# Kernel tuning notes

Hardware: AMD Instinct MI355X
Metric: run time of the kernel (lower is better)

Reference implementation:

```python
import jax, jax.numpy as jnp
import numpy as np

N_NODES = 100000
N_EDGES = 1600000
HID = 256
HEADS = 4
HEAD_DIM = HID // HEADS
EPS = 1e-5


def _layernorm(x, g, b):
    mu = jnp.mean(x, axis=-1, keepdims=True)
    var = jnp.mean(jnp.square(x - mu), axis=-1, keepdims=True)
    return (x - mu) * jax.lax.rsqrt(var + EPS) * g + b


def setup_inputs() -> dict:
    key = jax.random.key(0)
    ks = jax.random.split(key, 16)
    s = 0.05  # small init, mimics xavier gain=0.1
    inp = {
        'h': jax.random.normal(ks[0], (N_NODES, HID), jnp.float32),
        'src': jax.random.randint(ks[1], (N_EDGES,), 0, N_NODES, jnp.int32),
        'dst': jax.random.randint(ks[2], (N_EDGES,), 0, N_NODES, jnp.int32),
        'Wq': jax.random.normal(ks[3], (HID, HID), jnp.float32) * s,
        'bq': jnp.zeros((HID,), jnp.float32),
        'Wk': jax.random.normal(ks[4], (HID, HID), jnp.float32) * s,
        'bk': jnp.zeros((HID,), jnp.float32),
        'Wv': jax.random.normal(ks[5], (HID, HID), jnp.float32) * s,
        'bv': jnp.zeros((HID,), jnp.float32),
        'Wo': jax.random.normal(ks[6], (HID, HID), jnp.float32) * s,
        'bo': jnp.zeros((HID,), jnp.float32),
        'W1': jax.random.normal(ks[7], (HID, 2 * HID), jnp.float32) * s,
        'b1': jnp.zeros((2 * HID,), jnp.float32),
        'W2': jax.random.normal(ks[8], (2 * HID, HID), jnp.float32) * s,
        'b2': jnp.zeros((HID,), jnp.float32),
        'g1': jnp.ones((HID,), jnp.float32),
        'be1': jnp.zeros((HID,), jnp.float32),
        'g2': jnp.ones((HID,), jnp.float32),
        'be2': jnp.zeros((HID,), jnp.float32),
    }
    return inp


def reference(h, src, dst, Wq, bq, Wk, bk, Wv, bv, Wo, bo, W1, b1, W2, b2, g1, be1, g2, be2):
    N = h.shape[0]
    scale = HEAD_DIM ** -0.5
    h_norm = _layernorm(h, g1, be1)
    Q = (h_norm @ Wq + bq).reshape(N, HEADS, HEAD_DIM)
    K = (h_norm @ Wk + bk).reshape(N, HEADS, HEAD_DIM)
    V = (h_norm @ Wv + bv).reshape(N, HEADS, HEAD_DIM)

    # per-edge attention logits: q from dst, k from src  -> [E, heads]
    logits = jnp.einsum('ehd,ehd->eh', Q[dst], K[src]) * scale

    # edge softmax grouped by destination node (dgl.ops.edge_softmax)
    seg_max = jax.ops.segment_max(logits, dst, num_segments=N)  # [N, heads]
    e = jnp.exp(logits - seg_max[dst])
    seg_sum = jax.ops.segment_sum(e, dst, num_segments=N)
    w = e / seg_sum[dst]  # [E, heads]

    # message = V[src] * attn ; aggregate by sum over incoming edges
    msg = V[src] * w[:, :, None]  # [E, heads, head_dim]
    h_new = jax.ops.segment_sum(msg, dst, num_segments=N).reshape(N, HID)

    h_attn = h_new @ Wo + bo
    h = h + h_attn  # dropout is identity in eval
    h2 = _layernorm(h, g2, be2)
    ffn = jax.nn.relu(h2 @ W1 + b1) @ W2 + b2
    return h + ffn
```

## Files before the change

### kernel.cpp

```cpp
#include <hip/hip_runtime.h>
#include <hip/hip_bf16.h>

#define NN 100000
#define NE 1600000

typedef __attribute__((ext_vector_type(8))) short bf16x8;
typedef __attribute__((ext_vector_type(4))) float f32x4;
typedef __attribute__((ext_vector_type(2))) float f32x2;
typedef __attribute__((ext_vector_type(2))) unsigned int u32x2;
typedef __attribute__((ext_vector_type(4))) unsigned int u32x4;

__device__ __forceinline__ float bf2f(unsigned short u) {
    union { unsigned int i; float f; } c; c.i = ((unsigned int)u) << 16; return c.f;
}
__device__ __forceinline__ unsigned short f2bf(float f) {
    union { float f; unsigned int i; } c; c.f = f;
    unsigned int lsb = (c.i >> 16) & 1u;
    c.i += 0x7FFFu + lsb;
    return (unsigned short)(c.i >> 16);
}
__device__ __forceinline__ unsigned char f2fp8(float v) {
    return (unsigned char)(__builtin_amdgcn_cvt_pk_fp8_f32(v, v, 0, false) & 0xff);
}
__device__ __forceinline__ void gload_lds16(const void* g, void* l) {
    __builtin_amdgcn_global_load_lds(
        (const __attribute__((address_space(1))) void*)g,
        (__attribute__((address_space(3))) void*)l, 16, 0, 0);
}

__global__ __launch_bounds__(256) void ln_k(
    const float* __restrict__ x, const float* __restrict__ g,
    const float* __restrict__ b, unsigned short* __restrict__ y, int nrows)
{
    int w = threadIdx.x >> 6, lane = threadIdx.x & 63;
    int row = blockIdx.x * 4 + w;
    if (row >= nrows) return;
    const float4 xv = *(const float4*)(x + (size_t)row * 256 + lane * 4);
    float s  = xv.x + xv.y + xv.z + xv.w;
    float sq = xv.x*xv.x + xv.y*xv.y + xv.z*xv.z + xv.w*xv.w;
    #pragma unroll
    for (int m = 1; m < 64; m <<= 1) {
        s  += __shfl_xor(s,  m);
        sq += __shfl_xor(sq, m);
    }
    float mu  = s * (1.0f / 256.0f);
    float var = sq * (1.0f / 256.0f) - mu * mu;
    float r = rsqrtf(var + 1e-5f);
    float4 gv = *(const float4*)(g + lane * 4);
    float4 bv = *(const float4*)(b + lane * 4);
    ushort4 o;
    o.x = f2bf((xv.x - mu) * r * gv.x + bv.x);
    o.y = f2bf((xv.y - mu) * r * gv.y + bv.y);
    o.z = f2bf((xv.z - mu) * r * gv.z + bv.z);
    o.w = f2bf((xv.w - mu) * r * gv.w + bv.w);
    *(ushort4*)(y + (size_t)row * 256 + lane * 4) = o;
}

__global__ __launch_bounds__(256) void wconv_k(
    const float* __restrict__ W, unsigned short* __restrict__ Wt, int K, int N)
{
    __shared__ unsigned short tl[32][33];
    int bk = blockIdx.x * 32, bn = blockIdx.y * 32;
    int lx = threadIdx.x & 31, ly = threadIdx.x >> 5;
    #pragma unroll
    for (int r = 0; r < 32; r += 8)
        tl[ly + r][lx] = f2bf(W[(size_t)(bk + ly + r) * N + bn + lx]);
    __syncthreads();
    #pragma unroll
    for (int r = 0; r < 32; r += 8)
        Wt[(size_t)(bn + ly + r) * K + bk + lx] = tl[lx][ly + r];
}

__global__ void bcat_k(const float* __restrict__ a, const float* __restrict__ b,
                       const float* __restrict__ c, float* __restrict__ o)
{
    int t = threadIdx.x;
    o[t] = a[t]; o[256 + t] = b[t]; o[512 + t] = c[t];
}

template<int OMODE, bool RELU, bool RES>
__global__ __launch_bounds__(512) void mgemm_k(
    const unsigned short* __restrict__ A, const unsigned short* __restrict__ Wt,
    const float* __restrict__ bias, void* __restrict__ outv, void* __restrict__ out2,
    const float* __restrict__ res, int M, int N, int K)
{
    __shared__ __align__(16) char lds[49152];
    const int t = threadIdx.x;
    const int lane = t & 63;
    const int wid = t >> 6;
    const int wm = wid >> 2, wn = wid & 3;
    const int bm = blockIdx.y * 128, bn = blockIdx.x * 256;

    f32x4 acc[4][4] = {};

    const int ra_s = t >> 2;
    const int sa_s = (t & 3) ^ (ra_s & 3);
    const size_t arow = (size_t)min(bm + ra_s, M - 1) * K + sa_s * 8;
    const int rb0 = t >> 2;
    const int sb0 = (t & 3) ^ (rb0 & 3);
    const int rb1 = (512 + t) >> 2;
    const int sb1 = (t & 3) ^ (rb1 & 3);
    const size_t brow0 = (size_t)(bn + rb0) * K + sb0 * 8;
    const size_t brow1 = (size_t)(bn + rb1) * K + sb1 * 8;

    const int fr = lane & 15, fs = lane >> 4;
    const int rslot = fs ^ (fr & 3);

    const int KS = K >> 5;
    int cur = 0;
    {
        unsigned short* Ab = (unsigned short*)(lds);
        unsigned short* Bb = (unsigned short*)(lds + 16384);
        gload_lds16(A + arow, Ab + t * 8);
        gload_lds16(Wt + brow0, Bb + t * 8);
        gload_lds16(Wt + brow1, Bb + (512 + t) * 8);
    }
    for (int ks = 0; ks < KS; ++ks) {
        __syncthreads();
        if (ks + 1 < KS) {
            int k1 = (ks + 1) << 5;
            unsigned short* Ab = (unsigned short*)(lds + (cur ^ 1) * 8192);
            unsigned short* Bb = (unsigned short*)(lds + 16384 + (cur ^ 1) * 16384);
            gload_lds16(A + arow + k1, Ab + t * 8);
            gload_lds16(Wt + brow0 + k1, Bb + t * 8);
            gload_lds16(Wt + brow1 + k1, Bb + (512 + t) * 8);
        }
        const unsigned short* As = (const unsigned short*)(lds + cur * 8192);
        const unsigned short* Bs = (const unsigned short*)(lds + 16384 + cur * 16384);
        bf16x8 af[4], bf[4];
        #pragma unroll
        for (int fm = 0; fm < 4; ++fm)
            af[fm] = *(const bf16x8*)&As[(wm * 64 + fm * 16 + fr) * 32 + rslot * 8];
        #pragma unroll
        for (int fn = 0; fn < 4; ++fn)
            bf[fn] = *(const bf16x8*)&Bs[(wn * 64 + fn * 16 + fr) * 32 + rslot * 8];
        #pragma unroll
        for (int fm = 0; fm < 4; ++fm)
            #pragma unroll
            for (int fn = 0; fn < 4; ++fn)
                acc[fm][fn] = __builtin_amdgcn_mfma_f32_16x16x32_bf16(
                    af[fm], bf[fn], acc[fm][fn], 0, 0, 0);
        cur ^= 1;
    }
    __syncthreads();

    float* wl = (float*)(lds + wid * 4352);
    const int rr = lane >> 2;
    const int c4 = (lane & 3) * 16;
    const int qg = lane >> 4;
    #pragma unroll
    for (int fm = 0; fm < 4; ++fm) {
        #pragma unroll
        for (int fn = 0; fn < 4; ++fn)
            #pragma unroll
            for (int i = 0; i < 4; ++i)
                wl[(qg * 4 + i) * 68 + fn * 16 + fr] = acc[fm][fn][i];
        f32x4 v0 = *(const f32x4*)&wl[rr * 68 + c4 + 0];
        f32x4 v1 = *(const f32x4*)&wl[rr * 68 + c4 + 4];
        f32x4 v2 = *(const f32x4*)&wl[rr * 68 + c4 + 8];
        f32x4 v3 = *(const f32x4*)&wl[rr * 68 + c4 + 12];
        const int rowg = bm + wm * 64 + fm * 16 + rr;
        const int colg = bn + wn * 64 + c4;
        if (rowg < M) {
            f32x4 b0 = *(const f32x4*)&bias[colg + 0];
            f32x4 b1 = *(const f32x4*)&bias[colg + 4];
            f32x4 b2 = *(const f32x4*)&bias[colg + 8];
            f32x4 b3 = *(const f32x4*)&bias[colg + 12];
            v0 += b0; v1 += b1; v2 += b2; v3 += b3;
            if (RES) {
                const float* rp = res + (size_t)rowg * N + colg;
                v0 += *(const f32x4*)(rp + 0);
                v1 += *(const f32x4*)(rp + 4);
                v2 += *(const f32x4*)(rp + 8);
                v3 += *(const f32x4*)(rp + 12);
            }
            if (RELU) {
                #pragma unroll
                for (int j = 0; j < 4; ++j) {
                    v0[j] = fmaxf(v0[j], 0.f); v1[j] = fmaxf(v1[j], 0.f);
                    v2[j] = fmaxf(v2[j], 0.f); v3[j] = fmaxf(v3[j], 0.f);
                }
            }
            if (OMODE == 0) {
                float* op = (float*)outv + (size_t)rowg * N + colg;
                *(f32x4*)(op + 0) = v0; *(f32x4*)(op + 4) = v1;
                *(f32x4*)(op + 8) = v2; *(f32x4*)(op + 12) = v3;
            } else if (OMODE == 1) {
                unsigned short* op = (unsigned short*)outv + (size_t)rowg * N + colg;
                u32x4 pa, pb;
                pa.x = f2bf(v0[0]) | ((unsigned int)f2bf(v0[1]) << 16);
                pa.y = f2bf(v0[2]) | ((unsigned int)f2bf(v0[3]) << 16);
                pa.z = f2bf(v1[0]) | ((unsigned int)f2bf(v1[1]) << 16);
                pa.w = f2bf(v1[2]) | ((unsigned int)f2bf(v1[3]) << 16);
                pb.x = f2bf(v2[0]) | ((unsigned int)f2bf(v2[1]) << 16);
                pb.y = f2bf(v2[2]) | ((unsigned int)f2bf(v2[3]) << 16);
                pb.z = f2bf(v3[0]) | ((unsigned int)f2bf(v3[1]) << 16);
                pb.w = f2bf(v3[2]) | ((unsigned int)f2bf(v3[3]) << 16);
                *(u32x4*)(op + 0) = pa;
                *(u32x4*)(op + 8) = pb;
            } else {
                if (colg < 256) {
                    unsigned short* op = (unsigned short*)outv + (size_t)rowg * 256 + colg;
                    u32x4 pa, pb;
                    pa.x = f2bf(v0[0]) | ((unsigned int)f2bf(v0[1]) << 16);
                    pa.y = f2bf(v0[2]) | ((unsigned int)f2bf(v0[3]) << 16);
                    pa.z = f2bf(v1[0]) | ((unsigned int)f2bf(v1[1]) << 16);
                    pa.w = f2bf(v1[2]) | ((unsigned int)f2bf(v1[3]) << 16);
                    pb.x = f2bf(v2[0]) | ((unsigned int)f2bf(v2[1]) << 16);
                    pb.y = f2bf(v2[2]) | ((unsigned int)f2bf(v2[3]) << 16);
                    pb.z = f2bf(v3[0]) | ((unsigned int)f2bf(v3[1]) << 16);
                    pb.w = f2bf(v3[2]) | ((unsigned int)f2bf(v3[3]) << 16);
                    *(u32x4*)(op + 0) = pa;
                    *(u32x4*)(op + 8) = pb;
                } else {
                    u32x4 p8;
                    unsigned int w0, w1, w2, w3;
                    w0 = __builtin_amdgcn_cvt_pk_fp8_f32(v0[0], v0[1], 0, false);
                    w0 = __builtin_amdgcn_cvt_pk_fp8_f32(v0[2], v0[3], w0, true);
                    w1 = __builtin_amdgcn_cvt_pk_fp8_f32(v1[0], v1[1], 0, false);
                    w1 = __builtin_amdgcn_cvt_pk_fp8_f32(v1[2], v1[3], w1, true);
                    w2 = __builtin_amdgcn_cvt_pk_fp8_f32(v2[0], v2[1], 0, false);
                    w2 = __builtin_amdgcn_cvt_pk_fp8_f32(v2[2], v2[3], w2, true);
                    w3 = __builtin_amdgcn_cvt_pk_fp8_f32(v3[0], v3[1], 0, false);
                    w3 = __builtin_amdgcn_cvt_pk_fp8_f32(v3[2], v3[3], w3, true);
                    p8.x = w0; p8.y = w1; p8.z = w2; p8.w = w3;
                    *(u32x4*)((unsigned char*)out2 + (size_t)rowg * 512 + (colg - 256)) = p8;
                }
            }
        }
    }
}

__global__ void degcnt_k(const int* __restrict__ dst, int* __restrict__ deg, int E)
{
    int e = blockIdx.x * blockDim.x + threadIdx.x;
    if (e < E) atomicAdd(deg + dst[e], 1);
}

__global__ __launch_bounds__(1024) void scan_k(int* __restrict__ a, int n)
{
    __shared__ int wsum[16];
    __shared__ int carry;
    __shared__ int tot;
    int t = threadIdx.x, lane = t & 63, w = t >> 6;
    if (t == 0) carry = 0;
    __syncthreads();
    for (int base = 0; base < n; base += 1024) {
        int i = base + t;
        int v = (i < n) ? a[i] : 0;
        int s = v;
        #pragma unroll
        for (int d2 = 1; d2 < 64; d2 <<= 1) {
            int u = __shfl_up(s, d2);
            if (lane >= d2) s += u;
        }
        if (lane == 63) wsum[w] = s;
        __syncthreads();
        if (t == 0) {
            int run = 0;
            #pragma unroll
            for (int j = 0; j < 16; ++j) { int x = wsum[j]; wsum[j] = run; run += x; }
            tot = run;
        }
        __syncthreads();
        int excl = carry + wsum[w] + (s - v);
        if (i < n) a[i] = excl;
        __syncthreads();
        if (t == 0) carry += tot;
        __syncthreads();
    }
    if (threadIdx.x == 0) a[n] = carry;
}

__global__ void scatter_k(
    const int* __restrict__ dst, const int* __restrict__ srcarr,
    const int* __restrict__ off, int* __restrict__ cursor,
    int* __restrict__ csr, int E)
{
    int e = blockIdx.x * blockDim.x + threadIdx.x;
    if (e >= E) return;
    int d = dst[e];
    int pos = off[d] + atomicAdd(cursor + d, 1);
    csr[pos] = srcarr[e];
}

__global__ __launch_bounds__(256) void attn_k(
    const int* __restrict__ csr, const int* __restrict__ off,
    const unsigned short* __restrict__ Q, const unsigned char* __restrict__ KV8,
    unsigned short* __restrict__ hnew)
{
    int w = threadIdx.x >> 6, lane = threadIdx.x & 63;
    int n = blockIdx.x * 4 + w;
    if (n >= NN) return;
    int e0 = off[n], e1 = off[n + 1];

    u32x2 qr = __builtin_nontemporal_load((const u32x2*)(Q + (size_t)n * 256 + lane * 4));
    const float q0 = bf2f((unsigned short)(qr.x & 0xffff)) * 0.125f;
    const float q1 = bf2f((unsigned short)(qr.x >> 16))    * 0.125f;
    const float q2 = bf2f((unsigned short)(qr.y & 0xffff)) * 0.125f;
    const float q3 = bf2f((unsigned short)(qr.y >> 16))    * 0.125f;

    float s = 0.f;
    float a0 = 0.f, a1 = 0.f, a2 = 0.f, a3 = 0.f;

    int i = e0;
    for (; i + 7 < e1; i += 8) {
        int ns[8];
        #pragma unroll
        for (int j = 0; j < 8; ++j) ns[j] = csr[i + j];
        unsigned int kd[8], vd[8];
        #pragma unroll
        for (int j = 0; j < 8; ++j) {
            const unsigned char* r = KV8 + (size_t)ns[j] * 512 + lane * 4;
            kd[j] = *(const unsigned int*)r;
            vd[j] = *(const unsigned int*)(r + 256);
        }
        float l[8];
        #pragma unroll
        for (int j = 0; j < 8; ++j) {
            f32x2 ka = __builtin_amdgcn_cvt_pk_f32_fp8(kd[j], false);
            f32x2 kb = __builtin_amdgcn_cvt_pk_f32_fp8(kd[j], true);
            l[j] = q0 * ka.x + q1 * ka.y + q2 * kb.x + q3 * kb.y;
        }
        #pragma unroll
        for (int m2 = 1; m2 < 16; m2 <<= 1) {
            #pragma unroll
            for (int j = 0; j < 8; ++j) l[j] += __shfl_xor(l[j], m2);
        }
        #pragma unroll
        for (int j = 0; j < 8; ++j) {
            float p = __expf(l[j]);
            f32x2 va = __builtin_amdgcn_cvt_pk_f32_fp8(vd[j], false);
            f32x2 vb = __builtin_amdgcn_cvt_pk_f32_fp8(vd[j], true);
            s  += p;
            a0 += p * va.x; a1 += p * va.y;
            a2 += p * vb.x; a3 += p * vb.y;
        }
    }
    for (; i + 3 < e1; i += 4) {
        int ns[4];
        #pragma unroll
        for (int j = 0; j < 4; ++j) ns[j] = csr[i + j];
        unsigned int kd[4], vd[4];
        #pragma unroll
        for (int j = 0; j < 4; ++j) {
            const unsigned char* r = KV8 + (size_t)ns[j] * 512 + lane * 4;
            kd[j] = *(const unsigned int*)r;
            vd[j] = *(const unsigned int*)(r + 256);
        }
        float l[4];
        #pragma unroll
        for (int j = 0; j < 4; ++j) {
            f32x2 ka = __builtin_amdgcn_cvt_pk_f32_fp8(kd[j], false);
            f32x2 kb = __builtin_amdgcn_cvt_pk_f32_fp8(kd[j], true);
            l[j] = q0 * ka.x + q1 * ka.y + q2 * kb.x + q3 * kb.y;
        }
        #pragma unroll
        for (int m2 = 1; m2 < 16; m2 <<= 1) {
            #pragma unroll
            for (int j = 0; j < 4; ++j) l[j] += __shfl_xor(l[j], m2);
        }
        #pragma unroll
        for (int j = 0; j < 4; ++j) {
            float p = __expf(l[j]);
            f32x2 va = __builtin_amdgcn_cvt_pk_f32_fp8(vd[j], false);
            f32x2 vb = __builtin_amdgcn_cvt_pk_f32_fp8(vd[j], true);
            s  += p;
            a0 += p * va.x; a1 += p * va.y;
            a2 += p * vb.x; a3 += p * vb.y;
        }
    }
    for (; i < e1; ++i) {
        int n0 = csr[i];
        const unsigned char* r = KV8 + (size_t)n0 * 512 + lane * 4;
        unsigned int kd = *(const unsigned int*)r;
        unsigned int vd = *(const unsigned int*)(r + 256);
        f32x2 ka = __builtin_amdgcn_cvt_pk_f32_fp8(kd, false);
        f32x2 kb = __builtin_amdgcn_cvt_pk_f32_fp8(kd, true);
        float l0 = q0 * ka.x + q1 * ka.y + q2 * kb.x + q3 * kb.y;
        #pragma unroll
        for (int m2 = 1; m2 < 16; m2 <<= 1) l0 += __shfl_xor(l0, m2);
        float p = __expf(l0);
        f32x2 va = __builtin_amdgcn_cvt_pk_f32_fp8(vd, false);
        f32x2 vb = __builtin_amdgcn_cvt_pk_f32_fp8(vd, true);
        s  += p;
        a0 += p * va.x; a1 += p * va.y;
        a2 += p * vb.x; a3 += p * vb.y;
    }
    float inv = (e1 > e0) ? 1.0f / s : 0.f;
    u32x2 ov;
    ov.x = ((unsigned int)f2bf(a1 * inv) << 16) | f2bf(a0 * inv);
    ov.y = ((unsigned int)f2bf(a3 * inv) << 16) | f2bf(a2 * inv);
    __builtin_nontemporal_store(ov, (u32x2*)(hnew + (size_t)n * 256 + lane * 4));
}

extern "C" void kernel_launch(void* const* d_in, const int* in_sizes, int n_in,
                              void* d_out, int out_size, void* d_ws, size_t ws_size,
                              hipStream_t stream)
{
    if (n_in < 19) return;
    const float* h   = (const float*)d_in[0];
    const int*   src = (const int*)d_in[1];
    const int*   dst = (const int*)d_in[2];
    const float* Wq  = (const float*)d_in[3];
    const float* bq  = (const float*)d_in[4];
    const float* Wk  = (const float*)d_in[5];
    const float* bk  = (const float*)d_in[6];
    const float* Wv  = (const float*)d_in[7];
    const float* bv  = (const float*)d_in[8];
    const float* Wo  = (const float*)d_in[9];
    const float* bo  = (const float*)d_in[10];
    const float* W1  = (const float*)d_in[11];
    const float* b1  = (const float*)d_in[12];
    const float* W2  = (const float*)d_in[13];
    const float* b2  = (const float*)d_in[14];
    const float* g1  = (const float*)d_in[15];
    const float* be1 = (const float*)d_in[16];
    const float* g2  = (const float*)d_in[17];
    const float* be2 = (const float*)d_in[18];
    float* out = (float*)d_out;

    char* w = (char*)d_ws;
    unsigned short* hnormb = (unsigned short*)(w + 0);
    unsigned short* Qb     = (unsigned short*)(w + 51200000);
    unsigned char*  KV8    = (unsigned char*)(w + 102400000);
    int*            degoff = (int*)(w + 153600000);
    int*            cursor = (int*)(w + 154000384);
    int*            csr    = (int*)(w + 154400768);
    unsigned short* Wqkvt  = (unsigned short*)(w + 160800768);
    unsigned short* Wot    = (unsigned short*)(w + 161193984);
    unsigned short* W1t    = (unsigned short*)(w + 161325056);
    unsigned short* W2t    = (unsigned short*)(w + 161587200);
    float*          bqkv   = (float*)(w + 161849344);
    unsigned short* hnewb  = hnormb;
    unsigned short* h2nb   = hnormb;
    unsigned short* ffnmid = (unsigned short*)(w + 51200000);

    hipMemsetAsync(degoff, 0, 400384, stream);
    hipMemsetAsync(cursor, 0, 400384, stream);

    const int M = NN;
    dim3 blk(256);
    dim3 blk512(512);

    wconv_k<<<dim3(8, 8),  blk, 0, stream>>>(Wq, Wqkvt,             256, 256);
    wconv_k<<<dim3(8, 8),  blk, 0, stream>>>(Wk, Wqkvt + 256 * 256, 256, 256);
    wconv_k<<<dim3(8, 8),  blk, 0, stream>>>(Wv, Wqkvt + 512 * 256, 256, 256);
    wconv_k<<<dim3(8, 8),  blk, 0, stream>>>(Wo, Wot, 256, 256);
    wconv_k<<<dim3(8, 16), blk, 0, stream>>>(W1, W1t, 256, 512);
    wconv_k<<<dim3(16, 8), blk, 0, stream>>>(W2, W2t, 512, 256);
    bcat_k<<<dim3(1), blk, 0, stream>>>(bq, bk, bv, bqkv);

    degcnt_k<<<dim3((NE + 255) / 256), blk, 0, stream>>>(dst, degoff, NE);
    scan_k<<<dim3(1), dim3(1024), 0, stream>>>(degoff, NN);
    scatter_k<<<dim3((NE + 255) / 256), blk, 0, stream>>>(dst, src, degoff, cursor, csr, NE);

    ln_k<<<dim3((NN + 3) / 4), blk, 0, stream>>>(h, g1, be1, hnormb, NN);

    dim3 gq(768 / 256, (M + 127) / 128);
    mgemm_k<2, false, false><<<gq, blk512, 0, stream>>>(hnormb, Wqkvt, bqkv, Qb, KV8, nullptr, M, 768, 256);

    attn_k<<<dim3((NN + 3) / 4), blk, 0, stream>>>(csr, degoff, Qb, KV8, hnewb);

    dim3 go(256 / 256, (M + 127) / 128);
    mgemm_k<0, false, true><<<go, blk512, 0, stream>>>(hnewb, Wot, bo, out, nullptr, h, M, 256, 256);

    ln_k<<<dim3((NN + 3) / 4), blk, 0, stream>>>(out, g2, be2, h2nb, NN);

    dim3 g1x(512 / 256, (M + 127) / 128);
    mgemm_k<1, true, false><<<g1x, blk512, 0, stream>>>(h2nb, W1t, b1, ffnmid, nullptr, nullptr, M, 512, 256);
    mgemm_k<0, false, true><<<go, blk512, 0, stream>>>(ffnmid, W2t, b2, out, nullptr, out, M, 256, 512);
}
```

Before: 701.6 us.

## Fuse second LayerNorm into Wo GEMM epilogue and store residual as bf16

```diff
diff --git a/kernel.cpp b/kernel.cpp
--- a/kernel.cpp
+++ b/kernel.cpp
@@ -19,8 +19,13 @@
     c.i += 0x7FFFu + lsb;
     return (unsigned short)(c.i >> 16);
 }
-__device__ __forceinline__ unsigned char f2fp8(float v) {
-    return (unsigned char)(__builtin_amdgcn_cvt_pk_fp8_f32(v, v, 0, false) & 0xff);
+__device__ __forceinline__ u32x4 pack8bf(f32x4 a, f32x4 b) {
+    u32x4 p;
+    p.x = f2bf(a[0]) | ((unsigned int)f2bf(a[1]) << 16);
+    p.y = f2bf(a[2]) | ((unsigned int)f2bf(a[3]) << 16);
+    p.z = f2bf(b[0]) | ((unsigned int)f2bf(b[1]) << 16);
+    p.w = f2bf(b[2]) | ((unsigned int)f2bf(b[3]) << 16);
+    return p;
 }
 __device__ __forceinline__ void gload_lds16(const void* g, void* l) {
     __builtin_amdgcn_global_load_lds(
@@ -82,7 +87,8 @@
 __global__ __launch_bounds__(512) void mgemm_k(
     const unsigned short* __restrict__ A, const unsigned short* __restrict__ Wt,
     const float* __restrict__ bias, void* __restrict__ outv, void* __restrict__ out2,
-    const float* __restrict__ res, int M, int N, int K)
+    const void* __restrict__ res, const float* __restrict__ g, const float* __restrict__ be,
+    int M, int N, int K)
 {
     __shared__ __align__(16) char lds[49152];
     const int t = threadIdx.x;
@@ -145,9 +151,11 @@
     __syncthreads();
 
     float* wl = (float*)(lds + wid * 4352);
+    float* stats = (float*)(lds + 34816);
     const int rr = lane >> 2;
     const int c4 = (lane & 3) * 16;
     const int qg = lane >> 4;
+
     #pragma unroll
     for (int fm = 0; fm < 4; ++fm) {
         #pragma unroll
@@ -162,17 +170,30 @@
         const int rowg = bm + wm * 64 + fm * 16 + rr;
         const int colg = bn + wn * 64 + c4;
         if (rowg < M) {
-            f32x4 b0 = *(const f32x4*)&bias[colg + 0];
-            f32x4 b1 = *(const f32x4*)&bias[colg + 4];
-            f32x4 b2 = *(const f32x4*)&bias[colg + 8];
-            f32x4 b3 = *(const f32x4*)&bias[colg + 12];
-            v0 += b0; v1 += b1; v2 += b2; v3 += b3;
+            v0 += *(const f32x4*)&bias[colg + 0];
+            v1 += *(const f32x4*)&bias[colg + 4];
+            v2 += *(const f32x4*)&bias[colg + 8];
+            v3 += *(const f32x4*)&bias[colg + 12];
             if (RES) {
-                const float* rp = res + (size_t)rowg * N + colg;
-                v0 += *(const f32x4*)(rp + 0);
-                v1 += *(const f32x4*)(rp + 4);
-                v2 += *(const f32x4*)(rp + 8);
-                v3 += *(const f32x4*)(rp + 12);
+                if (OMODE == 4) {
+                    const unsigned short* rp = (const unsigned short*)res + (size_t)rowg * N + colg;
+                    u32x4 ra = *(const u32x4*)rp;
+                    u32x4 rb = *(const u32x4*)(rp + 8);
+                    v0[0] += bf2f(ra.x & 0xffff); v0[1] += bf2f(ra.x >> 16);
+                    v0[2] += bf2f(ra.y & 0xffff); v0[3] += bf2f(ra.y >> 16);
+                    v1[0] += bf2f(ra.z & 0xffff); v1[1] += bf2f(ra.z >> 16);
+                    v1[2] += bf2f(ra.w & 0xffff); v1[3] += bf2f(ra.w >> 16);
+                    v2[0] += bf2f(rb.x & 0xffff); v2[1] += bf2f(rb.x >> 16);
+                    v2[2] += bf2f(rb.y & 0xffff); v2[3] += bf2f(rb.y >> 16);
+                    v3[0] += bf2f(rb.z & 0xffff); v3[1] += bf2f(rb.z >> 16);
+                    v3[2] += bf2f(rb.w & 0xffff); v3[3] += bf2f(rb.w >> 16);
+                } else {
+                    const float* rp = (const float*)res + (size_t)rowg * N + colg;
+                    v0 += *(const f32x4*)(rp + 0);
+                    v1 += *(const f32x4*)(rp + 4);
+                    v2 += *(const f32x4*)(rp + 8);
+                    v3 += *(const f32x4*)(rp + 12);
+                }
             }
             if (RELU) {
                 #pragma unroll
@@ -181,37 +202,26 @@
                     v2[j] = fmaxf(v2[j], 0.f); v3[j] = fmaxf(v3[j], 0.f);
                 }
             }
-            if (OMODE == 0) {
+        } else {
+            v0 = 0.f; v1 = 0.f; v2 = 0.f; v3 = 0.f;
+        }
+
+        if (OMODE == 3) {
+            acc[fm][0] = v0; acc[fm][1] = v1; acc[fm][2] = v2; acc[fm][3] = v3;
+        } else if (rowg < M) {
+            if (OMODE == 0 || OMODE == 4) {
                 float* op = (float*)outv + (size_t)rowg * N + colg;
                 *(f32x4*)(op + 0) = v0; *(f32x4*)(op + 4) = v1;
                 *(f32x4*)(op + 8) = v2; *(f32x4*)(op + 12) = v3;
             } else if (OMODE == 1) {
                 unsigned short* op = (unsigned short*)outv + (size_t)rowg * N + colg;
-                u32x4 pa, pb;
-                pa.x = f2bf(v0[0]) | ((unsigned int)f2bf(v0[1]) << 16);
-                pa.y = f2bf(v0[2]) | ((unsigned int)f2bf(v0[3]) << 16);
-                pa.z = f2bf(v1[0]) | ((unsigned int)f2bf(v1[1]) << 16);
-                pa.w = f2bf(v1[2]) | ((unsigned int)f2bf(v1[3]) << 16);
-                pb.x = f2bf(v2[0]) | ((unsigned int)f2bf(v2[1]) << 16);
-                pb.y = f2bf(v2[2]) | ((unsigned int)f2bf(v2[3]) << 16);
-                pb.z = f2bf(v3[0]) | ((unsigned int)f2bf(v3[1]) << 16);
-                pb.w = f2bf(v3[2]) | ((unsigned int)f2bf(v3[3]) << 16);
-                *(u32x4*)(op + 0) = pa;
-                *(u32x4*)(op + 8) = pb;
+                *(u32x4*)(op + 0) = pack8bf(v0, v1);
+                *(u32x4*)(op + 8) = pack8bf(v2, v3);
             } else {
                 if (colg < 256) {
                     unsigned short* op = (unsigned short*)outv + (size_t)rowg * 256 + colg;
-                    u32x4 pa, pb;
-                    pa.x = f2bf(v0[0]) | ((unsigned int)f2bf(v0[1]) << 16);
-                    pa.y = f2bf(v0[2]) | ((unsigned int)f2bf(v0[3]) << 16);
-                    pa.z = f2bf(v1[0]) | ((unsigned int)f2bf(v1[1]) << 16);
-                    pa.w = f2bf(v1[2]) | ((unsigned int)f2bf(v1[3]) << 16);
-                    pb.x = f2bf(v2[0]) | ((unsigned int)f2bf(v2[1]) << 16);
-                    pb.y = f2bf(v2[2]) | ((unsigned int)f2bf(v2[3]) << 16);
-                    pb.z = f2bf(v3[0]) | ((unsigned int)f2bf(v3[1]) << 16);
-                    pb.w = f2bf(v3[2]) | ((unsigned int)f2bf(v3[3]) << 16);
-                    *(u32x4*)(op + 0) = pa;
-                    *(u32x4*)(op + 8) = pb;
+                    *(u32x4*)(op + 0) = pack8bf(v0, v1);
+                    *(u32x4*)(op + 8) = pack8bf(v2, v3);
                 } else {
                     u32x4 p8;
                     unsigned int w0, w1, w2, w3;
@@ -226,6 +236,56 @@
                     p8.x = w0; p8.y = w1; p8.z = w2; p8.w = w3;
                     *(u32x4*)((unsigned char*)out2 + (size_t)rowg * 512 + (colg - 256)) = p8;
                 }
+            }
+        }
+    }
+
+    if (OMODE == 3) {
+        #pragma unroll
+        for (int fm = 0; fm < 4; ++fm) {
+            float s = 0.f, q = 0.f;
+            #pragma unroll
+            for (int j = 0; j < 4; ++j)
+                #pragma unroll
+                for (int c = 0; c < 4; ++c) {
+                    float x = acc[fm][j][c];
+                    s += x; q += x * x;
+                }
+            s += __shfl_xor(s, 1); q += __shfl_xor(q, 1);
+            s += __shfl_xor(s, 2); q += __shfl_xor(q, 2);
+            if ((lane & 3) == 0) {
+                int rowl = wm * 64 + fm * 16 + rr;
+                stats[rowl * 8 + wn * 2 + 0] = s;
+                stats[rowl * 8 + wn * 2 + 1] = q;
+            }
+        }
+        __syncthreads();
+        #pragma unroll
+        for (int fm = 0; fm < 4; ++fm) {
+            const int rowl = wm * 64 + fm * 16 + rr;
+            const int rowg = bm + rowl;
+            float s = stats[rowl * 8 + 0] + stats[rowl * 8 + 2] + stats[rowl * 8 + 4] + stats[rowl * 8 + 6];
+            float q = stats[rowl * 8 + 1] + stats[rowl * 8 + 3] + stats[rowl * 8 + 5] + stats[rowl * 8 + 7];
+            float mu = s * (1.0f / 256.0f);
+            float var = q * (1.0f / 256.0f) - mu * mu;
+            float rstd = rsqrtf(var + 1e-5f);
+            const int colg = bn + wn * 64 + c4;
+            if (rowg < M) {
+                unsigned short* mp = (unsigned short*)out2 + (size_t)rowg * 256 + colg;
+                *(u32x4*)(mp + 0) = pack8bf(acc[fm][0], acc[fm][1]);
+                *(u32x4*)(mp + 8) = pack8bf(acc[fm][2], acc[fm][3]);
+                f32x4 nv[4];
+                #pragma unroll
+                for (int j = 0; j < 4; ++j) {
+                    f32x4 gv = *(const f32x4*)&g[colg + j * 4];
+                    f32x4 bv = *(const f32x4*)&be[colg + j * 4];
+                    #pragma unroll
+                    for (int c = 0; c < 4; ++c)
+                        nv[j][c] = (acc[fm][j][c] - mu) * rstd * gv[c] + bv[c];
+                }
+                unsigned short* op = (unsigned short*)outv + (size_t)rowg * 256 + colg;
+                *(u32x4*)(op + 0) = pack8bf(nv[0], nv[1]);
+                *(u32x4*)(op + 8) = pack8bf(nv[2], nv[3]);
             }
         }
     }
@@ -427,14 +487,15 @@
     int*            degoff = (int*)(w + 153600000);
     int*            cursor = (int*)(w + 154000384);
     int*            csr    = (int*)(w + 154400768);
-    unsigned short* Wqkvt  = (unsigned short*)(w + 160800768);
-    unsigned short* Wot    = (unsigned short*)(w + 161193984);
-    unsigned short* W1t    = (unsigned short*)(w + 161325056);
-    unsigned short* W2t    = (unsigned short*)(w + 161587200);
-    float*          bqkv   = (float*)(w + 161849344);
+    unsigned short* Wqkvt  = (unsigned short*)(w + 204800000);
+    unsigned short* Wot    = (unsigned short*)(w + 205193216);
+    unsigned short* W1t    = (unsigned short*)(w + 205324288);
+    unsigned short* W2t    = (unsigned short*)(w + 205586432);
+    float*          bqkv   = (float*)(w + 205848576);
     unsigned short* hnewb  = hnormb;
     unsigned short* h2nb   = hnormb;
-    unsigned short* ffnmid = (unsigned short*)(w + 51200000);
+    unsigned short* hmidb  = Qb;
+    unsigned short* ffnmid = (unsigned short*)(w + 102400000);
 
     hipMemsetAsync(degoff, 0, 400384, stream);
     hipMemsetAsync(cursor, 0, 400384, stream);
@@ -458,16 +519,14 @@
     ln_k<<<dim3((NN + 3) / 4), blk, 0, stream>>>(h, g1, be1, hnormb, NN);
 
     dim3 gq(768 / 256, (M + 127) / 128);
-    mgemm_k<2, false, false><<<gq, blk512, 0, stream>>>(hnormb, Wqkvt, bqkv, Qb, KV8, nullptr, M, 768, 256);
+    mgemm_k<2, false, false><<<gq, blk512, 0, stream>>>(hnormb, Wqkvt, bqkv, Qb, KV8, nullptr, nullptr, nullptr, M, 768, 256);
 
     attn_k<<<dim3((NN + 3) / 4), blk, 0, stream>>>(csr, degoff, Qb, KV8, hnewb);
 
-    dim3 go(256 / 256, (M + 127) / 128);
-    mgemm_k<0, false, true><<<go, blk512, 0, stream>>>(hnewb, Wot, bo, out, nullptr, h, M, 256, 256);
-
-    ln_k<<<dim3((NN + 3) / 4), blk, 0, stream>>>(out, g2, be2, h2nb, NN);
+    dim3 go(1, (M + 127) / 128);
+    mgemm_k<3, false, true><<<go, blk512, 0, stream>>>(hnewb, Wot, bo, h2nb, hmidb, h, g2, be2, M, 256, 256);
 
     dim3 g1x(512 / 256, (M + 127) / 128);
-    mgemm_k<1, true, false><<<g1x, blk512, 0, stream>>>(h2nb, W1t, b1, ffnmid, nullptr, nullptr, M, 512, 256);
-    mgemm_k<0, false, true><<<go, blk512, 0, stream>>>(ffnmid, W2t, b2, out, nullptr, out, M, 256, 512);
-}
+    mgemm_k<1, true, false><<<g1x, blk512, 0, stream>>>(h2nb, W1t, b1, ffnmid, nullptr, nullptr, nullptr, nullptr, M, 512, 256);
+    mgemm_k<4, false, true><<<go, blk512, 0, stream>>>(ffnmid, W2t, b2, out, nullptr, hmidb, nullptr, nullptr, M, 256, 512);
+}
```

After: 684.2 us. -2.5%, faster.
